# Optimization experiments

Measured on AMD Instinct MI355X. Metric: run time of the kernel, lower is better.

## Reference

```python
import jax, jax.numpy as jnp
import numpy as np

N, E, D, H = 50000, 800000, 128, 8
HD = D // H  # 16
HID = 512
EPS = 1e-5
SLOPE = 0.2  # DGL GATConv default negative_slope


def setup_inputs() -> dict:
    key = jax.random.key(0)
    ks = jax.random.split(key, 10)
    s = 0.1
    return {
        "x": jax.random.normal(ks[0], (N, D), jnp.float32),
        "src": jax.random.randint(ks[1], (E,), 0, N),
        "dst": jax.random.randint(ks[2], (E,), 0, N),
        "W": jax.random.normal(ks[3], (D, D), jnp.float32) * s,
        "attn_l": jax.random.normal(ks[4], (H, HD), jnp.float32) * s,
        "attn_r": jax.random.normal(ks[5], (H, HD), jnp.float32) * s,
        "bias_gat": jnp.zeros((D,), jnp.float32),
        "bn1_gamma": jnp.ones((D,), jnp.float32),
        "bn1_beta": jnp.zeros((D,), jnp.float32),
        "W1": jax.random.normal(ks[6], (D, HID), jnp.float32) * s,
        "b1": jnp.zeros((HID,), jnp.float32),
        "W2": jax.random.normal(ks[7], (HID, D), jnp.float32) * s,
        "b2": jnp.zeros((D,), jnp.float32),
        "bn2_gamma": jnp.ones((D,), jnp.float32),
        "bn2_beta": jnp.zeros((D,), jnp.float32),
    }


def _batchnorm(v, gamma, beta):
    # BatchNorm1d, training-mode forward (batch statistics, biased var)
    mu = v.mean(0)
    var = v.var(0)
    return (v - mu) * jax.lax.rsqrt(var + EPS) * gamma + beta


def reference(x, src, dst, W, attn_l, attn_r, bias_gat,
              bn1_gamma, bn1_beta, W1, b1, W2, b2, bn2_gamma, bn2_beta):
    n = x.shape[0]
    # GATConv: project + per-head attention logits
    feat = (x @ W).reshape(n, H, HD)                     # [N, H, hd]
    el = jnp.einsum('nhd,hd->nh', feat, attn_l)          # [N, H]
    er = jnp.einsum('nhd,hd->nh', feat, attn_r)          # [N, H]
    e = el[src] + er[dst]                                # [E, H]
    e = jnp.where(e > 0, e, SLOPE * e)                   # LeakyReLU
    # segment (edge) softmax over incoming edges of each dst node
    m = jax.ops.segment_max(e, dst, num_segments=n)      # [N, H]
    ee = jnp.exp(e - m[dst])
    denom = jax.ops.segment_sum(ee, dst, num_segments=n)
    alpha = ee / denom[dst]                              # [E, H]
    # weighted scatter-aggregate of source features
    msg = feat[src] * alpha[:, :, None]                  # [E, H, hd]
    agg = jax.ops.segment_sum(msg, dst, num_segments=n)  # [N, H, hd]
    h = agg.reshape(n, D) + bias_gat
    # BN -> Linear -> ReLU -> Linear -> BN
    h = _batchnorm(h, bn1_gamma, bn1_beta)
    h = jax.nn.relu(h @ W1 + b1) @ W2 + b2
    h = _batchnorm(h, bn2_gamma, bn2_beta)
    return h
```

## Files before the change

kernel.cpp:

```cpp
#include <hip/hip_runtime.h>
#include <math.h>

#define NHEAD 8
#define DD 128
#define HIDD 512
#define NB 768

typedef _Float16 half8 __attribute__((ext_vector_type(8)));
typedef _Float16 half4 __attribute__((ext_vector_type(4)));
typedef float floatx4 __attribute__((ext_vector_type(4)));

__device__ __forceinline__ int swz256(int row, int bytecol) {
  return row * 256 + (bytecol ^ ((row & 15) << 4));
}
__device__ __forceinline__ int swz512(int row, int bytecol) {
  return row * 512 + (bytecol ^ ((row & 15) << 4));
}

__global__ __launch_bounds__(256) void pack_kernel(
    const float* __restrict__ W, const float* __restrict__ W1,
    const float* __restrict__ W2, _Float16* __restrict__ WP,
    _Float16* __restrict__ W1TP, _Float16* __restrict__ W2P)
{
  int i = blockIdx.x * 256 + threadIdx.x;
  if (i < 4 * 128 * 4 * 8) {
    int ii = i & 7, l4 = (i >> 3) & 3, col = (i >> 5) & 127, kc = i >> 12;
    WP[i] = (_Float16)W[(kc * 32 + l4 * 8 + ii) * DD + col];
  }
  if (i < 65536) {
    int ii = i & 7, e = (i >> 3) & 63, tile = i >> 9;
    int l4 = e >> 4, l15 = e & 15, hb = tile >> 2, kc = tile & 3;
    W1TP[i] = (_Float16)W1[(size_t)(kc * 32 + l4 * 8 + ii) * HIDD + hb * 16 + l15];
  }
  if (i < 65536) {
    int ii = i & 7, e = (i >> 3) & 63, tile = i >> 9;
    int l4 = e >> 4, l15 = e & 15, c = tile >> 3, cb = tile & 7;
    int hidden = (ii < 4) ? (2 * c) * 16 + 4 * l4 + ii
                          : (2 * c + 1) * 16 + 4 * l4 + (ii - 4);
    W2P[i] = (_Float16)W2[(size_t)hidden * DD + cb * 16 + l15];
  }
}

__global__ __launch_bounds__(256) void feat_mfma_kernel(
    const float* __restrict__ x, const _Float16* __restrict__ WP,
    _Float16* __restrict__ feat16, int N, int T)
{
  __shared__ char xs[32 * 512];
  const int tid = threadIdx.x;
  const int wv = tid >> 6, lane = tid & 63;
  const int l15 = lane & 15, l4 = lane >> 4;
  const int row = tid >> 3, seg = tid & 7;

  int t = blockIdx.x;
  float4 pre[4];
  {
    const int n = t * 32 + row;
    const bool ok = (t < T) && (n < N);
    const float4* sp = (const float4*)(x + (size_t)n * DD + seg * 16);
    const float4 z = make_float4(0.f, 0.f, 0.f, 0.f);
    #pragma unroll
    for (int c = 0; c < 4; ++c) pre[c] = ok ? sp[c] : z;
  }

  for (; t < T; t += NB) {
    const int n0 = t * 32;
    #pragma unroll
    for (int c = 0; c < 4; ++c)
      *(float4*)(xs + swz512(row, seg * 64 + c * 16)) = pre[c];
    __syncthreads();

    floatx4 acc[2][2];
    #pragma unroll
    for (int mf = 0; mf < 2; ++mf) { acc[mf][0] = (floatx4)0.f; acc[mf][1] = (floatx4)0.f; }

    #pragma unroll
    for (int kc = 0; kc < 4; ++kc) {
      half8 b0 = *(const half8*)(WP + ((kc * 128 + wv * 32 + l15) * 4 + l4) * 8);
      half8 b1 = *(const half8*)(WP + ((kc * 128 + wv * 32 + 16 + l15) * 4 + l4) * 8);
      #pragma unroll
      for (int mf = 0; mf < 2; ++mf) {
        const int rr = mf * 16 + l15;
        float4 a0 = *(const float4*)(xs + swz512(rr, kc * 128 + l4 * 32));
        float4 a1 = *(const float4*)(xs + swz512(rr, kc * 128 + l4 * 32 + 16));
        half8 af;
        af[0] = (_Float16)a0.x; af[1] = (_Float16)a0.y; af[2] = (_Float16)a0.z; af[3] = (_Float16)a0.w;
        af[4] = (_Float16)a1.x; af[5] = (_Float16)a1.y; af[6] = (_Float16)a1.z; af[7] = (_Float16)a1.w;
        acc[mf][0] = __builtin_amdgcn_mfma_f32_16x16x32_f16(af, b0, acc[mf][0], 0, 0, 0);
        acc[mf][1] = __builtin_amdgcn_mfma_f32_16x16x32_f16(af, b1, acc[mf][1], 0, 0, 0);
      }
    }

    {
      const int tn = t + NB;
      const int n = tn * 32 + row;
      const bool ok = (tn < T) && (n < N);
      const float4* sp = (const float4*)(x + (size_t)n * DD + seg * 16);
      const float4 z = make_float4(0.f, 0.f, 0.f, 0.f);
      #pragma unroll
      for (int c = 0; c < 4; ++c) pre[c] = ok ? sp[c] : z;
    }

    #pragma unroll
    for (int mf = 0; mf < 2; ++mf) {
      #pragma unroll
      for (int r = 0; r < 4; ++r) {
        const int rown = n0 + mf * 16 + l4 * 4 + r;
        if (rown < N) {
          feat16[(size_t)rown * DD + wv * 32 + l15] = (_Float16)acc[mf][0][r];
          feat16[(size_t)rown * DD + wv * 32 + 16 + l15] = (_Float16)acc[mf][1][r];
        }
      }
    }
    __syncthreads();
  }
}

__global__ __launch_bounds__(256) void elr_kernel(
    const _Float16* __restrict__ feat16, const float* __restrict__ attn_l,
    const float* __restrict__ attn_r, float* __restrict__ el,
    float* __restrict__ er, int N)
{
  int gid = blockIdx.x * 256 + threadIdx.x;
  if (gid >= N * NHEAD) return;
  const int n = gid >> 3, h = gid & 7;
  const half8* fp = (const half8*)(feat16 + (size_t)n * DD + h * 16);
  half8 f0 = fp[0], f1 = fp[1];
  float sl = 0.f, sr = 0.f;
  #pragma unroll
  for (int d = 0; d < 8; ++d) {
    float v0 = (float)f0[d], v1 = (float)f1[d];
    sl = fmaf(v0, attn_l[h * 16 + d], sl);
    sl = fmaf(v1, attn_l[h * 16 + 8 + d], sl);
    sr = fmaf(v0, attn_r[h * 16 + d], sr);
    sr = fmaf(v1, attn_r[h * 16 + 8 + d], sr);
  }
  el[gid] = sl;
  er[gid] = sr;
}

__global__ __launch_bounds__(256) void count_kernel(const int* __restrict__ dst,
                                                    int* __restrict__ counts,
                                                    int* __restrict__ rank, int E)
{
  int e = blockIdx.x * 256 + threadIdx.x;
  if (e < E) rank[e] = atomicAdd(&counts[dst[e]], 1);
}

__global__ __launch_bounds__(256) void scan1_kernel(const int* __restrict__ counts,
                                                    int* __restrict__ offsets,
                                                    int* __restrict__ btot)
{
  __shared__ int wsum[4];
  const int lane = threadIdx.x & 63;
  const int wid = threadIdx.x >> 6;
  int4 c = *(const int4*)(counts + blockIdx.x * 1024 + threadIdx.x * 4);
  int q = c.x + c.y + c.z + c.w;
  int incl = q;
  #pragma unroll
  for (int d = 1; d < 64; d <<= 1) {
    int t = __shfl_up(incl, d, 64);
    if (lane >= d) incl += t;
  }
  if (lane == 63) wsum[wid] = incl;
  __syncthreads();
  int wprefix = 0;
  for (int w = 0; w < wid; ++w) wprefix += wsum[w];
  int excl = wprefix + incl - q;
  int4 o;
  o.x = excl; o.y = excl + c.x; o.z = o.y + c.y; o.w = o.z + c.z;
  *(int4*)(offsets + blockIdx.x * 1024 + threadIdx.x * 4) = o;
  if (threadIdx.x == 0) btot[blockIdx.x] = wsum[0] + wsum[1] + wsum[2] + wsum[3];
}

__global__ __launch_bounds__(64) void scan2_kernel(const int* __restrict__ btot,
                                                   int* __restrict__ bof, int nchunk)
{
  const int t = threadIdx.x;
  const int K = (nchunk + 63) >> 6;
  const int base = t * K;
  int s = 0;
  for (int i = 0; i < K; ++i) if (base + i < nchunk) s += btot[base + i];
  int incl = s;
  #pragma unroll
  for (int d = 1; d < 64; d <<= 1) {
    int tt = __shfl_up(incl, d, 64);
    if (t >= d) incl += tt;
  }
  int run = incl - s;
  for (int i = 0; i < K; ++i) if (base + i < nchunk) { bof[base + i] = run; run += btot[base + i]; }
}

__global__ __launch_bounds__(256) void fill_kernel(const int* __restrict__ src,
                                                   const int* __restrict__ dst,
                                                   const int* __restrict__ offsets,
                                                   const int* __restrict__ bof,
                                                   const int* __restrict__ rank,
                                                   int* __restrict__ srcl, int E)
{
  int e = blockIdx.x * 256 + threadIdx.x;
  if (e < E) {
    int d = dst[e];
    srcl[offsets[d] + bof[d >> 10] + rank[e]] = src[e];
  }
}

__global__ __launch_bounds__(256) void agg_kernel(
    const _Float16* __restrict__ feat16, const float* __restrict__ el,
    const float* __restrict__ er, const int* __restrict__ offsets,
    const int* __restrict__ bof, const int* __restrict__ srcl,
    const float* __restrict__ bias, float* __restrict__ hout, int N)
{
  int gid = blockIdx.x * 256 + threadIdx.x;
  if (gid >= N * 16) return;
  const int n = gid >> 4;
  const int sub = gid & 15;
  const int hh = sub >> 1;
  const int half = sub & 1;
  const int o0 = offsets[n] + bof[n >> 10];
  const int o1 = offsets[n + 1] + bof[(n + 1) >> 10];
  const int cnt = o1 - o0;
  const int mid = o0 + ((cnt + 1) >> 1);
  int j = half ? mid : o0;
  const int je = half ? o1 : mid;
  const float er_nh = er[n * NHEAD + hh];

  float s = 0.f;
  float a[16];
  #pragma unroll
  for (int d = 0; d < 16; ++d) a[d] = 0.f;

  for (; j + 3 < je; j += 4) {
    const int s0 = srcl[j], s1 = srcl[j + 1], s2 = srcl[j + 2], s3 = srcl[j + 3];
    float e0 = el[s0 * NHEAD + hh] + er_nh;
    float e1 = el[s1 * NHEAD + hh] + er_nh;
    float e2 = el[s2 * NHEAD + hh] + er_nh;
    float e3 = el[s3 * NHEAD + hh] + er_nh;
    const half8* f0p = (const half8*)(feat16 + (size_t)s0 * DD + hh * 16);
    const half8* f1p = (const half8*)(feat16 + (size_t)s1 * DD + hh * 16);
    const half8* f2p = (const half8*)(feat16 + (size_t)s2 * DD + hh * 16);
    const half8* f3p = (const half8*)(feat16 + (size_t)s3 * DD + hh * 16);
    e0 = e0 > 0.f ? e0 : 0.2f * e0;
    e1 = e1 > 0.f ? e1 : 0.2f * e1;
    e2 = e2 > 0.f ? e2 : 0.2f * e2;
    e3 = e3 > 0.f ? e3 : 0.2f * e3;
    const float p0 = __expf(e0), p1 = __expf(e1), p2 = __expf(e2), p3 = __expf(e3);
    half8 f00 = f0p[0], f01 = f0p[1];
    half8 f10 = f1p[0], f11 = f1p[1];
    half8 f20 = f2p[0], f21 = f2p[1];
    half8 f30 = f3p[0], f31 = f3p[1];
    s += (p0 + p1) + (p2 + p3);
    #pragma unroll
    for (int d = 0; d < 8; ++d) {
      float t0 = fmaf(p0, (float)f00[d], fmaf(p1, (float)f10[d], a[d]));
      a[d] = fmaf(p2, (float)f20[d], fmaf(p3, (float)f30[d], t0));
      float t1 = fmaf(p0, (float)f01[d], fmaf(p1, (float)f11[d], a[d + 8]));
      a[d + 8] = fmaf(p2, (float)f21[d], fmaf(p3, (float)f31[d], t1));
    }
  }
  for (; j < je; ++j) {
    const int s0 = srcl[j];
    float e0 = el[s0 * NHEAD + hh] + er_nh;
    e0 = e0 > 0.f ? e0 : 0.2f * e0;
    const float p0 = __expf(e0);
    const half8* f0p = (const half8*)(feat16 + (size_t)s0 * DD + hh * 16);
    half8 f00 = f0p[0], f01 = f0p[1];
    s += p0;
    #pragma unroll
    for (int d = 0; d < 8; ++d) {
      a[d]     = fmaf(p0, (float)f00[d], a[d]);
      a[d + 8] = fmaf(p0, (float)f01[d], a[d + 8]);
    }
  }

  s += __shfl_xor(s, 1, 64);
  #pragma unroll
  for (int d = 0; d < 16; ++d) a[d] += __shfl_xor(a[d], 1, 64);

  const float inv = (cnt > 0) ? 1.f / s : 0.f;
  const int cbase = hh * 16 + half * 8;
  float* op = hout + (size_t)n * DD + cbase;
  const float* bp = bias + cbase;
  const int abase = half * 8;
  float4 o0v, o1v;
  o0v.x = fmaf(a[abase + 0], inv, bp[0]);
  o0v.y = fmaf(a[abase + 1], inv, bp[1]);
  o0v.z = fmaf(a[abase + 2], inv, bp[2]);
  o0v.w = fmaf(a[abase + 3], inv, bp[3]);
  o1v.x = fmaf(a[abase + 4], inv, bp[4]);
  o1v.y = fmaf(a[abase + 5], inv, bp[5]);
  o1v.z = fmaf(a[abase + 6], inv, bp[6]);
  o1v.w = fmaf(a[abase + 7], inv, bp[7]);
  *(float4*)(op) = o0v;
  *(float4*)(op + 4) = o1v;
}

__global__ __launch_bounds__(256) void bnstats_kernel(
    const float* __restrict__ h, float* __restrict__ sums,
    float* __restrict__ sumsq, int N)
{
  __shared__ float rs[256], rss[256];
  const int c = threadIdx.x & 127;
  const int half = threadIdx.x >> 7;
  const int rowsPer = (N + gridDim.x - 1) / gridDim.x;
  const int r0 = blockIdx.x * rowsPer;
  const int r1 = min(N, r0 + rowsPer);
  float s = 0.f, ss = 0.f;
  for (int r = r0 + half; r < r1; r += 2) {
    float v = h[(size_t)r * DD + c];
    s += v; ss += v * v;
  }
  rs[threadIdx.x] = s; rss[threadIdx.x] = ss;
  __syncthreads();
  if (threadIdx.x < 128) {
    s = rs[threadIdx.x] + rs[threadIdx.x + 128];
    ss = rss[threadIdx.x] + rss[threadIdx.x + 128];
    atomicAdd(&sums[c], s);
    atomicAdd(&sumsq[c], ss);
  }
}

__global__ __launch_bounds__(256, 2) void mlp_mfma_kernel(
    const float* __restrict__ hbuf, const float* __restrict__ sum1,
    const float* __restrict__ ss1, const float* __restrict__ bn1_g,
    const float* __restrict__ bn1_b, const _Float16* __restrict__ W1TP,
    const _Float16* __restrict__ W2P, const float* __restrict__ b1,
    const float* __restrict__ b2, float* __restrict__ out, int N)
{
  __shared__ char myA[8192];
  __shared__ char xch[3 * 8192];
  const int tid = threadIdx.x;
  const int wv = tid >> 6;
  const int lane = tid & 63;
  const int l15 = lane & 15, l4 = lane >> 4;
  const int n0 = blockIdx.x * 32;
  if (n0 >= N) return;

  {
    const int c0 = (tid & 31) * 4;
    const int rq = tid >> 5;
    float sc[4], sh[4];
    #pragma unroll
    for (int jj = 0; jj < 4; ++jj) {
      float mean = sum1[c0 + jj] / (float)N;
      float var = ss1[c0 + jj] / (float)N - mean * mean;
      float s = bn1_g[c0 + jj] * rsqrtf(var + 1e-5f);
      sc[jj] = s; sh[jj] = bn1_b[c0 + jj] - mean * s;
    }
    #pragma unroll
    for (int it = 0; it < 4; ++it) {
      const int row = it * 8 + rq;
      const int n = n0 + row;
      float4 v = make_float4(0.f, 0.f, 0.f, 0.f);
      if (n < N) v = *(const float4*)(hbuf + (size_t)n * DD + c0);
      half4 hv;
      hv[0] = (_Float16)fmaf(v.x, sc[0], sh[0]);
      hv[1] = (_Float16)fmaf(v.y, sc[1], sh[1]);
      hv[2] = (_Float16)fmaf(v.z, sc[2], sh[2]);
      hv[3] = (_Float16)fmaf(v.w, sc[3], sh[3]);
      *(half4*)(myA + swz256(row, c0 * 2)) = hv;
    }
  }
  __syncthreads();

  half8 xf[2][4];
  #pragma unroll
  for (int nb = 0; nb < 2; ++nb)
    #pragma unroll
    for (int kc = 0; kc < 4; ++kc)
      xf[nb][kc] = *(const half8*)(myA + swz256(nb * 16 + l15, kc * 64 + l4 * 16));

  floatx4 acc2[2][8];
  #pragma unroll
  for (int nb = 0; nb < 2; ++nb)
    #pragma unroll
    for (int cb = 0; cb < 8; ++cb) acc2[nb][cb] = (floatx4)0.f;

  half8 a2s[4][2];
  #pragma unroll
  for (int c8 = 0; c8 < 4; ++c8) {
    const int c = wv * 4 + c8;
    floatx4 dA[2], dB[2];
    dA[0] = (floatx4)0.f; dA[1] = (floatx4)0.f;
    dB[0] = (floatx4)0.f; dB[1] = (floatx4)0.f;
    half8 wA[4], wB[4];
    #pragma unroll
    for (int kc = 0; kc < 4; ++kc) {
      wA[kc] = *(const half8*)(W1TP + (size_t)((2 * c) * 4 + kc) * 512 + (l4 * 16 + l15) * 8);
      wB[kc] = *(const half8*)(W1TP + (size_t)((2 * c + 1) * 4 + kc) * 512 + (l4 * 16 + l15) * 8);
    }
    __builtin_amdgcn_s_setprio(1);
    #pragma unroll
    for (int kc = 0; kc < 4; ++kc) {
      dA[0] = __builtin_amdgcn_mfma_f32_16x16x32_f16(wA[kc], xf[0][kc], dA[0], 0, 0, 0);
      dA[1] = __builtin_amdgcn_mfma_f32_16x16x32_f16(wA[kc], xf[1][kc], dA[1], 0, 0, 0);
      dB[0] = __builtin_amdgcn_mfma_f32_16x16x32_f16(wB[kc], xf[0][kc], dB[0], 0, 0, 0);
      dB[1] = __builtin_amdgcn_mfma_f32_16x16x32_f16(wB[kc], xf[1][kc], dB[1], 0, 0, 0);
    }
    __builtin_amdgcn_s_setprio(0);
    floatx4 bA = *(const floatx4*)&b1[(2 * c) * 16 + l4 * 4];
    floatx4 bB = *(const floatx4*)&b1[(2 * c + 1) * 16 + l4 * 4];
    #pragma unroll
    for (int nb = 0; nb < 2; ++nb) {
      #pragma unroll
      for (int r = 0; r < 4; ++r) {
        float vA = dA[nb][r] + bA[r];
        float vB = dB[nb][r] + bB[r];
        a2s[c8][nb][r]     = (_Float16)(vA > 0.f ? vA : 0.f);
        a2s[c8][nb][r + 4] = (_Float16)(vB > 0.f ? vB : 0.f);
      }
    }
  }
  #pragma unroll
  for (int c8 = 0; c8 < 4; ++c8) {
    const int c = wv * 4 + c8;
    half8 w2[8];
    #pragma unroll
    for (int cb = 0; cb < 8; ++cb)
      w2[cb] = *(const half8*)(W2P + (size_t)(c * 8 + cb) * 512 + (l4 * 16 + l15) * 8);
    __builtin_amdgcn_s_setprio(1);
    #pragma unroll
    for (int cb = 0; cb < 8; ++cb) {
      acc2[0][cb] = __builtin_amdgcn_mfma_f32_16x16x32_f16(a2s[c8][0], w2[cb], acc2[0][cb], 0, 0, 0);
      acc2[1][cb] = __builtin_amdgcn_mfma_f32_16x16x32_f16(a2s[c8][1], w2[cb], acc2[1][cb], 0, 0, 0);
    }
    __builtin_amdgcn_s_setprio(0);
  }

  if (wv != 0) {
    char* myX = xch + (wv - 1) * 8192;
    #pragma unroll
    for (int nb = 0; nb < 2; ++nb) {
      #pragma unroll
      for (int cb = 0; cb < 8; ++cb) {
        half4 hv;
        #pragma unroll
        for (int r = 0; r < 4; ++r) hv[r] = (_Float16)acc2[nb][cb][r];
        *(half4*)(myX + ((nb * 8 + cb) * 64 + lane) * 8) = hv;
      }
    }
  }
  __syncthreads();
  if (wv == 0) {
    float b2v[8];
    #pragma unroll
    for (int cb = 0; cb < 8; ++cb) b2v[cb] = b2[cb * 16 + l15];
    #pragma unroll
    for (int sw = 0; sw < 3; ++sw) {
      #pragma unroll
      for (int nb = 0; nb < 2; ++nb) {
        #pragma unroll
        for (int cb = 0; cb < 8; ++cb) {
          half4 hv = *(const half4*)(xch + sw * 8192 + ((nb * 8 + cb) * 64 + lane) * 8);
          #pragma unroll
          for (int r = 0; r < 4; ++r) acc2[nb][cb][r] += (float)hv[r];
        }
      }
    }
    #pragma unroll
    for (int nb = 0; nb < 2; ++nb) {
      #pragma unroll
      for (int r = 0; r < 4; ++r) {
        const int rown = n0 + nb * 16 + l4 * 4 + r;
        if (rown < N) {
          #pragma unroll
          for (int cb = 0; cb < 8; ++cb)
            out[(size_t)rown * DD + cb * 16 + l15] = acc2[nb][cb][r] + b2v[cb];
        }
      }
    }
  }
}

__global__ __launch_bounds__(256) void applybn_kernel(
    float* __restrict__ out, const float* __restrict__ sum2,
    const float* __restrict__ ss2, const float* __restrict__ gamma,
    const float* __restrict__ beta, int N, int total4)
{
  __shared__ float sc[128], sh[128];
  if (threadIdx.x < 128) {
    int c = threadIdx.x;
    float mean = sum2[c] / (float)N;
    float var = ss2[c] / (float)N - mean * mean;
    float s = gamma[c] * rsqrtf(var + 1e-5f);
    sc[c] = s;
    sh[c] = beta[c] - mean * s;
  }
  __syncthreads();
  int i = blockIdx.x * 256 + threadIdx.x;
  const int stride = gridDim.x * 256;
  for (; i < total4; i += stride) {
    float4 v = ((float4*)out)[i];
    int c = (i & 31) * 4;
    float4 scv = *(const float4*)&sc[c];
    float4 shv = *(const float4*)&sh[c];
    v.x = fmaf(v.x, scv.x, shv.x); v.y = fmaf(v.y, scv.y, shv.y);
    v.z = fmaf(v.z, scv.z, shv.z); v.w = fmaf(v.w, scv.w, shv.w);
    ((float4*)out)[i] = v;
  }
}

extern "C" void kernel_launch(void* const* d_in, const int* in_sizes, int n_in,
                              void* d_out, int out_size, void* d_ws, size_t ws_size,
                              hipStream_t stream) {
  const float* x        = (const float*)d_in[0];
  const int*   src      = (const int*)d_in[1];
  const int*   dst      = (const int*)d_in[2];
  const float* W        = (const float*)d_in[3];
  const float* attn_l   = (const float*)d_in[4];
  const float* attn_r   = (const float*)d_in[5];
  const float* bias_gat = (const float*)d_in[6];
  const float* bn1_g    = (const float*)d_in[7];
  const float* bn1_b    = (const float*)d_in[8];
  const float* W1       = (const float*)d_in[9];
  const float* b1       = (const float*)d_in[10];
  const float* W2       = (const float*)d_in[11];
  const float* b2       = (const float*)d_in[12];
  const float* bn2_g    = (const float*)d_in[13];
  const float* bn2_b    = (const float*)d_in[14];
  float* out = (float*)d_out;

  const int N = in_sizes[0] / DD;
  const int E = in_sizes[1];
  const int NPAD = ((N + 1023) / 1024) * 1024;
  const int NCHUNK = NPAD / 1024;
  const int T = (N + 31) / 32;

  _Float16* feat16 = (_Float16*)d_ws;
  float* hbuf = (float*)(feat16 + (size_t)((N + 1) & ~1) * DD);
  float* el   = hbuf + (size_t)N * DD;
  float* er   = el + (size_t)N * NHEAD;
  int* counts = (int*)(er + (size_t)N * NHEAD);
  int* offsets = counts + NPAD;
  int* srcl   = offsets + NPAD;
  int* btot   = srcl + E;
  int* bof    = btot + 64;
  float* stats = (float*)(bof + 64);
  float* sum1 = stats, *ss1 = stats + 128;
  float* sum2 = stats + 256, *ss2 = stats + 384;
  _Float16* WP   = (_Float16*)(stats + 1024);
  _Float16* W1TP = WP + 4 * 128 * 32;
  _Float16* W2P  = W1TP + 65536;
  int* rank = (int*)hbuf;

  hipMemsetAsync(counts, 0, (size_t)NPAD * sizeof(int), stream);
  hipMemsetAsync(stats, 0, 512 * sizeof(float), stream);

  pack_kernel<<<256, 256, 0, stream>>>(W, W1, W2, WP, W1TP, W2P);
  feat_mfma_kernel<<<NB, 256, 0, stream>>>(x, WP, feat16, N, T);
  elr_kernel<<<(N * NHEAD + 255) / 256, 256, 0, stream>>>(feat16, attn_l, attn_r, el, er, N);
  count_kernel<<<(E + 255) / 256, 256, 0, stream>>>(dst, counts, rank, E);
  scan1_kernel<<<NCHUNK, 256, 0, stream>>>(counts, offsets, btot);
  scan2_kernel<<<1, 64, 0, stream>>>(btot, bof, NCHUNK);
  fill_kernel<<<(E + 255) / 256, 256, 0, stream>>>(src, dst, offsets, bof, rank, srcl, E);
  agg_kernel<<<(N * 16 + 255) / 256, 256, 0, stream>>>(feat16, el, er, offsets, bof,
                                                       srcl, bias_gat, hbuf, N);
  bnstats_kernel<<<256, 256, 0, stream>>>(hbuf, sum1, ss1, N);
  mlp_mfma_kernel<<<T, 256, 0, stream>>>(hbuf, sum1, ss1, bn1_g, bn1_b, W1TP, W2P,
                                         b1, b2, out, N);
  bnstats_kernel<<<256, 256, 0, stream>>>(out, sum2, ss2, N);
  applybn_kernel<<<2048, 256, 0, stream>>>(out, sum2, ss2, bn2_g, bn2_b, N, N * DD / 4);
}
```

Measured before the change: 231.3 us.

## Store features and attention logits head-major so gathers stay head-local

The projected features and the el/er logits are now stored per head ([H][NR][16] and [H][NR]) instead of node-major. The aggregation grid is reorganised so each block handles one head over 128 destination nodes. Concurrent blocks then gather from a 1.6 MB per-head slice, which is meant to improve L2 locality for the random source gathers. The cost is less coalesced stores in the feature GEMM epilogue, and each destination's offsets are now read once per head.

```diff
diff --git a/kernel.cpp b/kernel.cpp
--- a/kernel.cpp
+++ b/kernel.cpp
@@ -43,7 +43,7 @@
 
 __global__ __launch_bounds__(256) void feat_mfma_kernel(
     const float* __restrict__ x, const _Float16* __restrict__ WP,
-    _Float16* __restrict__ feat16, int N, int T)
+    _Float16* __restrict__ featT, int N, int NR, int T)
 {
   __shared__ char xs[32 * 512];
   const int tid = threadIdx.x;
@@ -106,8 +106,8 @@
       for (int r = 0; r < 4; ++r) {
         const int rown = n0 + mf * 16 + l4 * 4 + r;
         if (rown < N) {
-          feat16[(size_t)rown * DD + wv * 32 + l15] = (_Float16)acc[mf][0][r];
-          feat16[(size_t)rown * DD + wv * 32 + 16 + l15] = (_Float16)acc[mf][1][r];
+          featT[((size_t)(wv * 2) * NR + rown) * 16 + l15]     = (_Float16)acc[mf][0][r];
+          featT[((size_t)(wv * 2 + 1) * NR + rown) * 16 + l15] = (_Float16)acc[mf][1][r];
         }
       }
     }
@@ -116,15 +116,16 @@
 }
 
 __global__ __launch_bounds__(256) void elr_kernel(
-    const _Float16* __restrict__ feat16, const float* __restrict__ attn_l,
-    const float* __restrict__ attn_r, float* __restrict__ el,
-    float* __restrict__ er, int N)
-{
-  int gid = blockIdx.x * 256 + threadIdx.x;
-  if (gid >= N * NHEAD) return;
-  const int n = gid >> 3, h = gid & 7;
-  const half8* fp = (const half8*)(feat16 + (size_t)n * DD + h * 16);
-  half8 f0 = fp[0], f1 = fp[1];
+    const _Float16* __restrict__ featT, const float* __restrict__ attn_l,
+    const float* __restrict__ attn_r, float* __restrict__ elT,
+    float* __restrict__ erT, int N, int NR)
+{
+  const int n = blockIdx.x * 256 + threadIdx.x;
+  const int h = blockIdx.y;
+  if (n >= N) return;
+  const _Float16* fp = featT + ((size_t)h * NR + n) * 16;
+  half8 f0 = *(const half8*)fp;
+  half8 f1 = *(const half8*)(fp + 8);
   float sl = 0.f, sr = 0.f;
   #pragma unroll
   for (int d = 0; d < 8; ++d) {
@@ -134,8 +135,8 @@
     sr = fmaf(v0, attn_r[h * 16 + d], sr);
     sr = fmaf(v1, attn_r[h * 16 + 8 + d], sr);
   }
-  el[gid] = sl;
-  er[gid] = sr;
+  elT[(size_t)h * NR + n] = sl;
+  erT[(size_t)h * NR + n] = sr;
 }
 
 __global__ __launch_bounds__(256) void count_kernel(const int* __restrict__ dst,
@@ -205,24 +206,26 @@
 }
 
 __global__ __launch_bounds__(256) void agg_kernel(
-    const _Float16* __restrict__ feat16, const float* __restrict__ el,
-    const float* __restrict__ er, const int* __restrict__ offsets,
+    const _Float16* __restrict__ featT, const float* __restrict__ elT,
+    const float* __restrict__ erT, const int* __restrict__ offsets,
     const int* __restrict__ bof, const int* __restrict__ srcl,
-    const float* __restrict__ bias, float* __restrict__ hout, int N)
-{
-  int gid = blockIdx.x * 256 + threadIdx.x;
-  if (gid >= N * 16) return;
-  const int n = gid >> 4;
-  const int sub = gid & 15;
-  const int hh = sub >> 1;
-  const int half = sub & 1;
+    const float* __restrict__ bias, float* __restrict__ hout, int N, int NR)
+{
+  const int h = blockIdx.x & 7;
+  const int nb = blockIdx.x >> 3;
+  const int tid = threadIdx.x;
+  const int n = nb * 128 + (tid >> 1);
+  if (n >= N) return;
+  const int half = tid & 1;
   const int o0 = offsets[n] + bof[n >> 10];
   const int o1 = offsets[n + 1] + bof[(n + 1) >> 10];
   const int cnt = o1 - o0;
   const int mid = o0 + ((cnt + 1) >> 1);
   int j = half ? mid : o0;
   const int je = half ? o1 : mid;
-  const float er_nh = er[n * NHEAD + hh];
+  const float er_nh = erT[(size_t)h * NR + n];
+  const float* elh = elT + (size_t)h * NR;
+  const _Float16* fh = featT + (size_t)h * NR * 16;
 
   float s = 0.f;
   float a[16];
@@ -231,14 +234,14 @@
 
   for (; j + 3 < je; j += 4) {
     const int s0 = srcl[j], s1 = srcl[j + 1], s2 = srcl[j + 2], s3 = srcl[j + 3];
-    float e0 = el[s0 * NHEAD + hh] + er_nh;
-    float e1 = el[s1 * NHEAD + hh] + er_nh;
-    float e2 = el[s2 * NHEAD + hh] + er_nh;
-    float e3 = el[s3 * NHEAD + hh] + er_nh;
-    const half8* f0p = (const half8*)(feat16 + (size_t)s0 * DD + hh * 16);
-    const half8* f1p = (const half8*)(feat16 + (size_t)s1 * DD + hh * 16);
-    const half8* f2p = (const half8*)(feat16 + (size_t)s2 * DD + hh * 16);
-    const half8* f3p = (const half8*)(feat16 + (size_t)s3 * DD + hh * 16);
+    float e0 = elh[s0] + er_nh;
+    float e1 = elh[s1] + er_nh;
+    float e2 = elh[s2] + er_nh;
+    float e3 = elh[s3] + er_nh;
+    const half8* f0p = (const half8*)(fh + (size_t)s0 * 16);
+    const half8* f1p = (const half8*)(fh + (size_t)s1 * 16);
+    const half8* f2p = (const half8*)(fh + (size_t)s2 * 16);
+    const half8* f3p = (const half8*)(fh + (size_t)s3 * 16);
     e0 = e0 > 0.f ? e0 : 0.2f * e0;
     e1 = e1 > 0.f ? e1 : 0.2f * e1;
     e2 = e2 > 0.f ? e2 : 0.2f * e2;
@@ -259,10 +262,10 @@
   }
   for (; j < je; ++j) {
     const int s0 = srcl[j];
-    float e0 = el[s0 * NHEAD + hh] + er_nh;
+    float e0 = elh[s0] + er_nh;
     e0 = e0 > 0.f ? e0 : 0.2f * e0;
     const float p0 = __expf(e0);
-    const half8* f0p = (const half8*)(feat16 + (size_t)s0 * DD + hh * 16);
+    const half8* f0p = (const half8*)(fh + (size_t)s0 * 16);
     half8 f00 = f0p[0], f01 = f0p[1];
     s += p0;
     #pragma unroll
@@ -277,7 +280,7 @@
   for (int d = 0; d < 16; ++d) a[d] += __shfl_xor(a[d], 1, 64);
 
   const float inv = (cnt > 0) ? 1.f / s : 0.f;
-  const int cbase = hh * 16 + half * 8;
+  const int cbase = h * 16 + half * 8;
   float* op = hout + (size_t)n * DD + cbase;
   const float* bp = bias + cbase;
   const int abase = half * 8;
@@ -524,12 +527,13 @@
   const int NPAD = ((N + 1023) / 1024) * 1024;
   const int NCHUNK = NPAD / 1024;
   const int T = (N + 31) / 32;
-
-  _Float16* feat16 = (_Float16*)d_ws;
-  float* hbuf = (float*)(feat16 + (size_t)((N + 1) & ~1) * DD);
-  float* el   = hbuf + (size_t)N * DD;
-  float* er   = el + (size_t)N * NHEAD;
-  int* counts = (int*)(er + (size_t)N * NHEAD);
+  const int NR = T * 32;
+
+  _Float16* featT = (_Float16*)d_ws;
+  float* hbuf = (float*)(featT + (size_t)NR * DD);
+  float* elT  = hbuf + (size_t)N * DD;
+  float* erT  = elT + (size_t)8 * NR;
+  int* counts = (int*)(erT + (size_t)8 * NR);
   int* offsets = counts + NPAD;
   int* srcl   = offsets + NPAD;
   int* btot   = srcl + E;
@@ -546,14 +550,17 @@
   hipMemsetAsync(stats, 0, 512 * sizeof(float), stream);
 
   pack_kernel<<<256, 256, 0, stream>>>(W, W1, W2, WP, W1TP, W2P);
-  feat_mfma_kernel<<<NB, 256, 0, stream>>>(x, WP, feat16, N, T);
-  elr_kernel<<<(N * NHEAD + 255) / 256, 256, 0, stream>>>(feat16, attn_l, attn_r, el, er, N);
+  feat_mfma_kernel<<<NB, 256, 0, stream>>>(x, WP, featT, N, NR, T);
+  {
+    dim3 g((N + 255) / 256, NHEAD);
+    elr_kernel<<<g, 256, 0, stream>>>(featT, attn_l, attn_r, elT, erT, N, NR);
+  }
   count_kernel<<<(E + 255) / 256, 256, 0, stream>>>(dst, counts, rank, E);
   scan1_kernel<<<NCHUNK, 256, 0, stream>>>(counts, offsets, btot);
   scan2_kernel<<<1, 64, 0, stream>>>(btot, bof, NCHUNK);
   fill_kernel<<<(E + 255) / 256, 256, 0, stream>>>(src, dst, offsets, bof, rank, srcl, E);
-  agg_kernel<<<(N * 16 + 255) / 256, 256, 0, stream>>>(feat16, el, er, offsets, bof,
-                                                       srcl, bias_gat, hbuf, N);
+  agg_kernel<<<((N + 127) / 128) * NHEAD, 256, 0, stream>>>(featT, elT, erT, offsets, bof,
+                                                            srcl, bias_gat, hbuf, N, NR);
   bnstats_kernel<<<256, 256, 0, stream>>>(hbuf, sum1, ss1, N);
   mlp_mfma_kernel<<<T, 256, 0, stream>>>(hbuf, sum1, ss1, bn1_g, bn1_b, W1TP, W2P,
                                          b1, b2, out, N);
```

Result: slower. 255.2 us (+10.4%).
